# Optimization experiments

Hardware: AMD Instinct MI355X
Metric: run time of the kernel (lower is better)

The kernel has to match this reference:

```python
import jax, jax.numpy as jnp
import numpy as np

B, E, S = 2, 1024, 2048
H = 16
D_QK = D_V = D_OUT = 1024
NEG = -1e4


def setup_inputs() -> dict:
    key = jax.random.key(0)
    ks = jax.random.split(key, 12)
    q = jax.random.normal(ks[0], (B, E, 1, S), jnp.float32)
    k = jax.random.normal(ks[1], (B, E, 1, S), jnp.float32)
    v = jax.random.normal(ks[2], (B, E, 1, S), jnp.float32)
    # causal qk_mask: (B, src, 1, tgt); src index > tgt index is masked
    causal = jnp.where(jnp.arange(S)[:, None] > jnp.arange(S)[None, :], NEG, 0.0).astype(jnp.float32)
    qk_mask = jnp.broadcast_to(causal[None, :, None, :], (B, S, 1, S))
    k_mask = jnp.zeros((B, S, 1, 1), jnp.float32)
    sc = 1.0 / np.sqrt(E)
    Wq = jax.random.normal(ks[3], (D_QK, E), jnp.float32) * sc
    Wk = jax.random.normal(ks[4], (D_QK, E), jnp.float32) * sc
    Wv = jax.random.normal(ks[5], (D_V, E), jnp.float32) * sc
    Wo = jax.random.normal(ks[6], (D_OUT, D_V), jnp.float32) * sc
    bq = jnp.zeros((D_QK,), jnp.float32)
    bk = jnp.zeros((D_QK,), jnp.float32)
    bv = jnp.zeros((D_V,), jnp.float32)
    bo = jnp.zeros((D_OUT,), jnp.float32)
    return {"q": q, "k": k, "v": v, "qk_mask": qk_mask, "k_mask": k_mask,
            "Wq": Wq, "bq": bq, "Wk": Wk, "bk": bk, "Wv": Wv, "bv": bv,
            "Wo": Wo, "bo": bo}


def reference(q, k, v, qk_mask, k_mask, Wq, bq, Wk, bk, Wv, bv, Wo, bo):
    b, _, _, tq = q.shape
    sk = k.shape[3]
    d_qk, d_v = Wq.shape[0], Wv.shape[0]
    dh, dvh = d_qk // H, d_v // H
    fact = float(dh) ** (-0.5)
    # 1x1 conv projections on (B, C, 1, S) == matmul over channels
    qp = jnp.einsum('oc,bcis->bois', Wq, q) + bq[None, :, None, None]
    kp = jnp.einsum('oc,bcis->bois', Wk, k) + bk[None, :, None, None]
    vp = jnp.einsum('oc,bcis->bois', Wv, v) + bv[None, :, None, None]
    # split heads: channel dim is head-major (contiguous chunks)
    qh = qp[:, :, 0, :].reshape(b, H, dh, tq)
    kh = kp[:, :, 0, :].reshape(b, H, dh, sk)
    vh = vp[:, :, 0, :].reshape(b, H, dvh, sk)
    # scores: (B, H, src, tgt); masks broadcast over heads
    scores = jnp.einsum('bhcq,bhck->bhkq', qh, kh) * fact
    scores = scores + qk_mask[:, None, :, 0, :] + k_mask[:, None, :, 0, 0][..., None]
    w = jax.nn.softmax(scores, axis=2)  # softmax over src (k) axis
    attn = jnp.einsum('bhkq,bhck->bhcq', w, vh).reshape(b, d_v, 1, tq)
    out = jnp.einsum('oc,bcis->bois', Wo, attn) + bo[None, :, None, None]
    return out
```

## Files before the change

### kernel.cpp

```cpp
#include <hip/hip_runtime.h>
#include <hip/hip_bf16.h>
#include <stdint.h>

typedef unsigned short u16;
typedef __attribute__((ext_vector_type(8))) short short8;
typedef __attribute__((ext_vector_type(4))) short short4v;
typedef __attribute__((ext_vector_type(4))) float f32x4;

#define MFMA16(a,b,c) __builtin_amdgcn_mfma_f32_16x16x32_bf16((a),(b),(c),0,0,0)
#define EXP2F(x) __builtin_amdgcn_exp2f(x)

typedef const __attribute__((address_space(1))) void glb_void;
typedef __attribute__((address_space(3))) void lds_void;

__device__ __forceinline__ u16 f2b(float f){
  unsigned u = __float_as_uint(f);
  u += 0x7fffu + ((u>>16)&1u);
  return (u16)(u>>16);
}
__device__ __forceinline__ unsigned pack_bf16(float a, float b){
  __hip_bfloat162 h = __float22bfloat162_rn(make_float2(a,b));
  unsigned u; __builtin_memcpy(&u, &h, 4); return u;
}
__device__ __forceinline__ void gld16(const void* g, void* l){
  __builtin_amdgcn_global_load_lds((glb_void*)g, (lds_void*)l, 16, 0, 0);
}

__device__ __forceinline__ void stage128x64_sw(const u16* g, u16* lds, int gstride, int w, int lane){
  const int sub = lane>>3, c16 = lane&7;
  const int gcol = (c16 ^ sub)<<3;
  #pragma unroll
  for (int i=0;i<4;++i){
    int r0 = (w*4+i)*8;
    gld16(g + (size_t)(r0 + sub)*gstride + gcol, lds + r0*64);
  }
}
__device__ __forceinline__ void stage64x64_sw(const u16* g, u16* lds, int gstride, int w, int lane){
  const int sub = lane>>3, c16 = lane&7;
  const int gcol = (c16 ^ sub)<<3;
  #pragma unroll
  for (int i=0;i<2;++i){
    int r0 = (w*2+i)*8;
    gld16(g + (size_t)(r0 + sub)*gstride + gcol, lds + r0*64);
  }
}
__device__ __forceinline__ const short8* frag64(const u16* lds, int row, int c16){
  return (const short8*)(lds + row*64 + ((c16 ^ (row&7))<<3));
}
__device__ __forceinline__ const short8* frag128(const u16* lds, int row, int c16){
  return (const short8*)(lds + row*128 + ((c16 ^ (row&15))<<3));
}

__global__ __launch_bounds__(256) void prep(
    const float* __restrict__ q, const float* __restrict__ k, const float* __restrict__ v,
    const float* __restrict__ qkm, const float* __restrict__ km,
    const float* __restrict__ Wq, const float* __restrict__ Wk,
    const float* __restrict__ Wv, const float* __restrict__ Wo,
    u16* __restrict__ W16, char* __restrict__ classes,
    u16* __restrict__ qT, u16* __restrict__ kT, u16* __restrict__ vT)
{
  __shared__ __align__(16) float t[64][72];
  const int bx = blockIdx.x, tid = threadIdx.x;
  const int S = 2048, E = 1024, nW = E*E;

  if (bx < 2048){
    const int sel = bx>>9, blk = bx&511;
    const float* src = sel==0?Wq : sel==1?Wk : sel==2?Wv : Wo;
    const float sc = (sel==0) ? 0.18033688f : 1.0f;
    u16* dst = W16 + (size_t)sel*nW;
    int i = (blk*256 + tid)*8;
    float4 a = *(const float4*)(src+i);
    float4 b = *(const float4*)(src+i+4);
    short8 o;
    o[0]=(short)f2b(a.x*sc); o[1]=(short)f2b(a.y*sc); o[2]=(short)f2b(a.z*sc); o[3]=(short)f2b(a.w*sc);
    o[4]=(short)f2b(b.x*sc); o[5]=(short)f2b(b.y*sc); o[6]=(short)f2b(b.z*sc); o[7]=(short)f2b(b.w*sc);
    *(short8*)(dst+i) = o;
  } else if (bx < 4096){
    const int tt = bx - 2048;
    const int b = tt>>10, qi = (tt>>5)&31, ki = tt&31;
    const int k0 = ki*64, q0 = qi*64;
    int az = 1, an = 1;
    #pragma unroll
    for (int p=0;p<4;++p){
      int e = tid + p*256;
      int row = e>>4, c4 = (e&15)*4;
      float kmv = km[(size_t)b*S + k0 + row];
      float4 mv = *(const float4*)&qkm[((size_t)b*S + k0 + row)*S + q0 + c4];
      mv.x += kmv; mv.y += kmv; mv.z += kmv; mv.w += kmv;
      az &= (mv.x==0.f) & (mv.y==0.f) & (mv.z==0.f) & (mv.w==0.f);
      an &= (mv.x<-1e3f) & (mv.y<-1e3f) & (mv.z<-1e3f) & (mv.w<-1e3f);
    }
    const int az_all = __syncthreads_and(az);
    const int an_all = __syncthreads_and(an);
    if (tid==0)
      classes[((size_t)b*32 + qi)*32 + ki] = an_all ? 2 : (az_all ? 0 : 1);
  } else {
    const int tt = bx - 4096;
    const int tensor = tt>>10, r = tt&1023;
    const int b = r>>9, rr = r&511;
    const int c0 = (rr>>5)*64, s0 = (rr&31)*64;
    const float* x = tensor==0 ? q : tensor==1 ? k : v;
    u16* xt = tensor==0 ? qT : tensor==1 ? kT : vT;
    #pragma unroll
    for (int p=0;p<4;++p){
      int e = tid + p*256;
      int row = e>>4, c4 = (e&15)*4;
      *(float4*)&t[row][c4] = *(const float4*)&x[((size_t)b*E + c0 + row)*S + s0 + c4];
    }
    __syncthreads();
    #pragma unroll
    for (int p=0;p<2;++p){
      int e = tid + p*256;
      int row = e>>3, col8 = (e&7)*8;
      short8 o;
      #pragma unroll
      for (int u=0;u<8;++u) o[u] = (short)f2b(t[col8+u][row]);
      *(short8*)&xt[((size_t)b*S + s0 + row)*E + c0 + col8] = o;
    }
  }
}

template<bool F32OUT>
__device__ __forceinline__ void gemm_core(
    const u16* __restrict__ A, const u16* __restrict__ Bt, const float* __restrict__ bias,
    float bscale, void* __restrict__ Cv, size_t cbase, int N, int K, int bias_on_m,
    int m0, int n0, u16* As, u16* Bs)
{
  const int tid = threadIdx.x, w = tid>>6, lane = tid&63;
  const int ln = lane&15, quad = lane>>4;
  const int m0w = (w>>1)*64, n0w = (w&1)*64;
  f32x4 acc[4][4];
  #pragma unroll
  for(int i=0;i<4;++i)
    #pragma unroll
    for(int j=0;j<4;++j) acc[i][j] = f32x4{0.f,0.f,0.f,0.f};

  for (int kc=0; kc<K; kc+=64){
    __syncthreads();
    stage128x64_sw(A  + (size_t)m0*K + kc, As, K, w, lane);
    stage128x64_sw(Bt + (size_t)n0*K + kc, Bs, K, w, lane);
    __syncthreads();
    #pragma unroll
    for (int kk=0; kk<64; kk+=32){
      const int c16 = (kk>>3) + quad;
      short8 af[4], bf[4];
      #pragma unroll
      for (int mt=0;mt<4;++mt) af[mt] = *frag64(As, m0w+mt*16+ln, c16);
      #pragma unroll
      for (int nt=0;nt<4;++nt) bf[nt] = *frag64(Bs, n0w+nt*16+ln, c16);
      #pragma unroll
      for (int mt=0;mt<4;++mt)
        #pragma unroll
        for (int nt=0;nt<4;++nt)
          acc[mt][nt] = MFMA16(af[mt], bf[nt], acc[mt][nt]);
    }
  }
  #pragma unroll
  for (int mt=0;mt<4;++mt){
    #pragma unroll
    for (int nt=0;nt<4;++nt){
      const int col = n0 + n0w + nt*16 + ln;
      const float bn = bias_on_m ? 0.f : bias[col]*bscale;
      #pragma unroll
      for (int r=0;r<4;++r){
        const int row = m0 + m0w + mt*16 + quad*4 + r;
        const float bb = bias_on_m ? bias[row]*bscale : bn;
        const float val = acc[mt][nt][r] + bb;
        const size_t idx = cbase + (size_t)row*N + col;
        if (F32OUT) ((float*)Cv)[idx] = val;
        else        ((u16*)Cv)[idx]   = f2b(val);
      }
    }
  }
}

__global__ __launch_bounds__(256,3) void proj(
    const u16* __restrict__ qT, const u16* __restrict__ kT, const u16* __restrict__ vT,
    const u16* __restrict__ W16,
    const float* __restrict__ bq, const float* __restrict__ bk, const float* __restrict__ bv,
    u16* __restrict__ Qb, u16* __restrict__ Kb, u16* __restrict__ Vb)
{
  __shared__ __align__(16) u16 As[128*64];
  __shared__ __align__(16) u16 Bs[128*64];
  const int bx = blockIdx.x;
  const int zone = bx>>7, r = bx&127;
  const size_t sSE = (size_t)2048*1024;
  const int nW = 1024*1024;
  if (zone < 4){
    const int sel = zone>>1, b = zone&1;
    const int m0 = (r>>3)*128, n0 = (r&7)*128;
    gemm_core<false>((sel? kT : qT) + b*sSE, W16 + (size_t)sel*nW, sel? bk : bq,
                     sel? 1.0f : 0.18033688f, sel? Kb : Qb, b*sSE,
                     1024, 1024, 0, m0, n0, As, Bs);
  } else {
    const int b = zone&1;
    const int m0 = (r>>4)*128, n0 = (r&15)*128;
    gemm_core<false>(W16 + (size_t)2*nW, vT + b*sSE, bv,
                     1.0f, Vb, b*sSE,
                     2048, 1024, 1, m0, n0, As, Bs);
  }
}

__global__ __launch_bounds__(256,4) void gemm_out64(
    const u16* __restrict__ Wo16, const u16* __restrict__ At, const float* __restrict__ bo,
    float* __restrict__ out)
{
  __shared__ __align__(16) u16 As[64*64];
  __shared__ __align__(16) u16 Bs[128*64];
  const int b = blockIdx.z;
  const int m0 = blockIdx.y*64, n0 = blockIdx.x*128;
  const size_t sSE = (size_t)2048*1024;
  const int K = 1024, N = 2048;
  const u16* Bt = At + b*sSE;
  const int tid = threadIdx.x, w = tid>>6, lane = tid&63;
  const int ln = lane&15, quad = lane>>4;
  const int m0w = (w>>1)*32, n0w = (w&1)*64;
  f32x4 acc[2][4];
  #pragma unroll
  for(int i=0;i<2;++i)
    #pragma unroll
    for(int j=0;j<4;++j) acc[i][j] = f32x4{0.f,0.f,0.f,0.f};

  for (int kc=0; kc<K; kc+=64){
    __syncthreads();
    stage64x64_sw (Wo16 + (size_t)m0*K + kc, As, K, w, lane);
    stage128x64_sw(Bt   + (size_t)n0*K + kc, Bs, K, w, lane);
    __syncthreads();
    #pragma unroll
    for (int kk=0; kk<64; kk+=32){
      const int c16 = (kk>>3) + quad;
      short8 af[2], bf[4];
      #pragma unroll
      for (int mt=0;mt<2;++mt) af[mt] = *frag64(As, m0w+mt*16+ln, c16);
      #pragma unroll
      for (int nt=0;nt<4;++nt) bf[nt] = *frag64(Bs, n0w+nt*16+ln, c16);
      #pragma unroll
      for (int mt=0;mt<2;++mt)
        #pragma unroll
        for (int nt=0;nt<4;++nt)
          acc[mt][nt] = MFMA16(af[mt], bf[nt], acc[mt][nt]);
    }
  }
  #pragma unroll
  for (int mt=0;mt<2;++mt){
    #pragma unroll
    for (int nt=0;nt<4;++nt){
      const int col = n0 + n0w + nt*16 + ln;
      #pragma unroll
      for (int r=0;r<4;++r){
        const int row = m0 + m0w + mt*16 + quad*4 + r;
        out[b*sSE + (size_t)row*N + col] = acc[mt][nt][r] + bo[row];
      }
    }
  }
}

__global__ __launch_bounds__(512,4) void attn(
    const u16* __restrict__ Qb, const u16* __restrict__ Kb, const u16* __restrict__ Vb,
    const float* __restrict__ qk_mask, const float* __restrict__ k_mask,
    const char* __restrict__ classes, u16* __restrict__ Ot)
{
  __shared__ __align__(16) u16 Ks[128*64];
  __shared__ __align__(16) u16 Vs[64*128];
  const int x = blockIdx.x;
  const int b = x&1, h = (x>>1)&15;
  const int pp = x>>5, pair = pp>>1, half = pp&1;
  const int tid = threadIdx.x, w = tid>>6, lane = tid&63;
  const int group = w>>2, wq = w&3;
  const int ln = lane&15, quad = lane>>4;
  const int S = 2048;
  const float LOG2E = 1.44269504f, C2 = 16.0f;

  const int qtA = 15-pair, qtB = pair;
  const int qt = group ? qtB : qtA;
  const int qg = qt*128 + half*64 + wq*16 + ln;
  short8 qf[2];
  #pragma unroll
  for (int kkI=0;kkI<2;++kkI)
    qf[kkI] = *(const short8*)&Qb[((size_t)b*S + qg)*1024 + h*64 + kkI*32 + quad*8];

  const char* clA = classes + ((size_t)b*32 + qtA*2 + half)*32;
  const char* clB = classes + ((size_t)b*32 + qtB*2 + half)*32;
  const char* cl  = group ? clB : clA;

  unsigned mA=0, mB=0;
  #pragma unroll
  for (int kt=0;kt<16;++kt){
    if (!((clA[2*kt]==2) & (clA[2*kt+1]==2))) mA |= 1u<<kt;
    if (!((clB[2*kt]==2) & (clB[2*kt+1]==2))) mB |= 1u<<kt;
  }
  const unsigned mS = mA|mB;
  const unsigned mMe = group ? mB : mA;

  float rs = 0.f;
  f32x4 acc[4];
  #pragma unroll
  for (int ct=0;ct<4;++ct) acc[ct] = f32x4{0.f,0.f,0.f,0.f};

  const u16* gK = Kb + ((size_t)b*S)*1024 + h*64;
  const u16* gV = Vb + ((size_t)b*1024 + h*64)*S;
  const int subK = lane>>3, cK = ((lane&7)^subK)<<3;
  const int subV = lane>>4, cV0 = lane&15;

  short8 kreg[2], vreg[2];
  auto issue = [&](int kt){
    const int k0 = kt*128;
    #pragma unroll
    for (int i=0;i<2;++i){
      const int r = (w*2+i)*8 + subK;
      kreg[i] = *(const short8*)(gK + (size_t)(k0 + r)*1024 + cK);
    }
    #pragma unroll
    for (int i=0;i<2;++i){
      const int row = (w*2+i)*4 + subV;
      vreg[i] = *(const short8*)(gV + (size_t)row*S + k0 + ((cV0 ^ (row&15))<<3));
    }
  };
  auto write_lds = [&](){
    #pragma unroll
    for (int i=0;i<2;++i)
      *(short8*)&Ks[(w*2+i)*512 + lane*8] = kreg[i];
    #pragma unroll
    for (int i=0;i<2;++i)
      *(short8*)&Vs[(w*2+i)*512 + lane*8] = vreg[i];
  };

  auto compute = [&](int kt){
    const char c0 = cl[2*kt], c1 = cl[2*kt+1];
    const bool nomask = (c0|c1)==0;
    const int k0 = kt*128;
    unsigned pk[8][2];
    #pragma unroll
    for (int t=0;t<8;++t){
      f32x4 s = f32x4{0.f,0.f,0.f,0.f};
      #pragma unroll
      for (int kkI=0;kkI<2;++kkI)
        s = MFMA16(*frag64(Ks, t*16+ln, kkI*4 + quad), qf[kkI], s);
      float e[4];
      if (nomask){
        #pragma unroll
        for (int r=0;r<4;++r) e[r] = EXP2F(s[r] - C2);
      } else {
        #pragma unroll
        for (int r=0;r<4;++r){
          const int kg = k0 + t*16 + quad*4 + r;
          const float m = qk_mask[((size_t)b*S + kg)*S + qg] + k_mask[(size_t)b*S + kg];
          e[r] = EXP2F(fmaf(m, LOG2E, s[r]) - C2);
        }
      }
      rs += (e[0]+e[1]) + (e[2]+e[3]);
      pk[t][0] = pack_bf16(e[0], e[1]);
      pk[t][1] = pack_bf16(e[2], e[3]);
    }
    const int srcA = (quad&1)*32 + ln, srcB = srcA + 16;
    const bool hi = (quad>>1)&1;
    #pragma unroll
    for (int c=0;c<4;++c){
      unsigned a0 = __shfl((int)pk[2*c][0],   srcA, 64);
      unsigned a1 = __shfl((int)pk[2*c][1],   srcA, 64);
      unsigned a2 = __shfl((int)pk[2*c][0],   srcB, 64);
      unsigned a3 = __shfl((int)pk[2*c][1],   srcB, 64);
      unsigned b0 = __shfl((int)pk[2*c+1][0], srcA, 64);
      unsigned b1 = __shfl((int)pk[2*c+1][1], srcA, 64);
      unsigned b2 = __shfl((int)pk[2*c+1][0], srcB, 64);
      unsigned b3 = __shfl((int)pk[2*c+1][1], srcB, 64);
      short8 pf;
      ((unsigned*)&pf)[0] = hi ? b0 : a0;
      ((unsigned*)&pf)[1] = hi ? b1 : a1;
      ((unsigned*)&pf)[2] = hi ? b2 : a2;
      ((unsigned*)&pf)[3] = hi ? b3 : a3;
      __builtin_amdgcn_s_setprio(1);
      #pragma unroll
      for (int ct=0;ct<4;++ct)
        acc[ct] = MFMA16(*frag128(Vs, ct*16+ln, c*4 + quad), pf, acc[ct]);
      __builtin_amdgcn_s_setprio(0);
    }
  };

  int cur = mS ? (__ffs(mS)-1) : 16;
  if (cur < 16) issue(cur);
  while (cur < 16){
    const unsigned above = mS & (0xfffffffeu << cur);
    const int nxt = above ? (__ffs(above)-1) : 16;
    __builtin_amdgcn_s_barrier();
    __builtin_amdgcn_sched_barrier(0);
    write_lds();
    if (nxt < 16) issue(nxt);
    asm volatile("s_waitcnt lgkmcnt(0)" ::: "memory");
    __builtin_amdgcn_s_barrier();
    __builtin_amdgcn_sched_barrier(0);
    if ((mMe>>cur)&1) compute(cur);
    cur = nxt;
  }

  rs += __shfl_xor(rs, 16, 64);
  rs += __shfl_xor(rs, 32, 64);
  const float rinv = 1.0f / rs;
  #pragma unroll
  for (int ct=0;ct<4;++ct){
    short4v o4;
    #pragma unroll
    for (int r=0;r<4;++r) o4[r] = (short)f2b(acc[ct][r] * rinv);
    *(short4v*)&Ot[((size_t)b*S + qg)*1024 + h*64 + ct*16 + quad*4] = o4;
  }
}

extern "C" void kernel_launch(void* const* d_in, const int* in_sizes, int n_in,
                              void* d_out, int out_size, void* d_ws, size_t ws_size,
                              hipStream_t stream)
{
  const float* q   = (const float*)d_in[0];
  const float* k   = (const float*)d_in[1];
  const float* v   = (const float*)d_in[2];
  const float* qkm = (const float*)d_in[3];
  const float* km  = (const float*)d_in[4];
  const float* Wq  = (const float*)d_in[5];
  const float* bq  = (const float*)d_in[6];
  const float* Wk  = (const float*)d_in[7];
  const float* bk  = (const float*)d_in[8];
  const float* Wv  = (const float*)d_in[9];
  const float* bv  = (const float*)d_in[10];
  const float* Wo  = (const float*)d_in[11];
  const float* bo  = (const float*)d_in[12];
  float* out = (float*)d_out;

  const size_t nAct = (size_t)2*2048*1024;
  const int   nW   = 1024*1024;

  u16* A0 = (u16*)d_ws;
  u16* A1 = A0 + nAct;
  u16* A2 = A1 + nAct;
  u16* A3 = A2 + nAct;
  u16* A4 = A3 + nAct;
  u16* A5 = A4 + nAct;
  u16* W16 = A5 + nAct;
  char* classes = (char*)(W16 + (size_t)4*nW);
  u16* Wo16 = W16 + (size_t)3*nW;

  dim3 blk(256);
  prep      <<<dim3(7168), blk, 0, stream>>>(q, k, v, qkm, km, Wq, Wk, Wv, Wo,
                                             W16, classes, A0, A1, A2);
  proj      <<<dim3(768),  blk, 0, stream>>>(A0, A1, A2, W16, bq, bk, bv, A3, A4, A5);
  attn      <<<dim3(512),  dim3(512), 0, stream>>>(A3, A4, A5, qkm, km, classes, A0);
  gemm_out64<<<dim3(16,16,2), blk, 0, stream>>>(Wo16, A0, bo, out);
}
```

Baseline: 258.7 us.

## Split attention into one 64-query strip per 256-thread block, heaviest first

Replaces the paired causal-balancing scheme, where a 512-thread block handled two query tiles (early and late) that shared K/V loads, with 1024 smaller 256-thread blocks. Each block handles one 64-query strip and is launched in descending order of work so the longest strips start first. Each block now loads only the K/V tiles it needs and skips the idle-wave iterations of the old paired scheme. In exchange, K/V tiles are no longer shared between paired tiles, so each thread issues twice as many loads per tile and there are more blocks to schedule.

```diff
diff --git a/kernel.cpp b/kernel.cpp
--- a/kernel.cpp
+++ b/kernel.cpp
@@ -255,42 +255,33 @@
   }
 }
 
-__global__ __launch_bounds__(512,4) void attn(
+__global__ __launch_bounds__(256,4) void attn(
     const u16* __restrict__ Qb, const u16* __restrict__ Kb, const u16* __restrict__ Vb,
     const float* __restrict__ qk_mask, const float* __restrict__ k_mask,
     const char* __restrict__ classes, u16* __restrict__ Ot)
 {
   __shared__ __align__(16) u16 Ks[128*64];
   __shared__ __align__(16) u16 Vs[64*128];
-  const int x = blockIdx.x;
-  const int b = x&1, h = (x>>1)&15;
-  const int pp = x>>5, pair = pp>>1, half = pp&1;
+  const int bx = blockIdx.x;
+  const int st = 31 - (bx>>5);
+  const int bh = bx & 31;
+  const int b = bh & 1, h = bh >> 1;
   const int tid = threadIdx.x, w = tid>>6, lane = tid&63;
-  const int group = w>>2, wq = w&3;
   const int ln = lane&15, quad = lane>>4;
   const int S = 2048;
   const float LOG2E = 1.44269504f, C2 = 16.0f;
 
-  const int qtA = 15-pair, qtB = pair;
-  const int qt = group ? qtB : qtA;
-  const int qg = qt*128 + half*64 + wq*16 + ln;
+  const int qg = st*64 + w*16 + ln;
   short8 qf[2];
   #pragma unroll
   for (int kkI=0;kkI<2;++kkI)
     qf[kkI] = *(const short8*)&Qb[((size_t)b*S + qg)*1024 + h*64 + kkI*32 + quad*8];
 
-  const char* clA = classes + ((size_t)b*32 + qtA*2 + half)*32;
-  const char* clB = classes + ((size_t)b*32 + qtB*2 + half)*32;
-  const char* cl  = group ? clB : clA;
-
-  unsigned mA=0, mB=0;
-  #pragma unroll
-  for (int kt=0;kt<16;++kt){
-    if (!((clA[2*kt]==2) & (clA[2*kt+1]==2))) mA |= 1u<<kt;
-    if (!((clB[2*kt]==2) & (clB[2*kt+1]==2))) mB |= 1u<<kt;
-  }
-  const unsigned mS = mA|mB;
-  const unsigned mMe = group ? mB : mA;
+  const char* cl = classes + ((size_t)b*32 + st)*32;
+  unsigned mMe=0;
+  #pragma unroll
+  for (int kt=0;kt<16;++kt)
+    if (!((cl[2*kt]==2) & (cl[2*kt+1]==2))) mMe |= 1u<<kt;
 
   float rs = 0.f;
   f32x4 acc[4];
@@ -302,27 +293,27 @@
   const int subK = lane>>3, cK = ((lane&7)^subK)<<3;
   const int subV = lane>>4, cV0 = lane&15;
 
-  short8 kreg[2], vreg[2];
+  short8 kreg[4], vreg[4];
   auto issue = [&](int kt){
     const int k0 = kt*128;
     #pragma unroll
-    for (int i=0;i<2;++i){
-      const int r = (w*2+i)*8 + subK;
+    for (int i=0;i<4;++i){
+      const int r = (w*4+i)*8 + subK;
       kreg[i] = *(const short8*)(gK + (size_t)(k0 + r)*1024 + cK);
     }
     #pragma unroll
-    for (int i=0;i<2;++i){
-      const int row = (w*2+i)*4 + subV;
+    for (int i=0;i<4;++i){
+      const int row = (w*4+i)*4 + subV;
       vreg[i] = *(const short8*)(gV + (size_t)row*S + k0 + ((cV0 ^ (row&15))<<3));
     }
   };
   auto write_lds = [&](){
     #pragma unroll
-    for (int i=0;i<2;++i)
-      *(short8*)&Ks[(w*2+i)*512 + lane*8] = kreg[i];
-    #pragma unroll
-    for (int i=0;i<2;++i)
-      *(short8*)&Vs[(w*2+i)*512 + lane*8] = vreg[i];
+    for (int i=0;i<4;++i)
+      *(short8*)&Ks[(w*4+i)*512 + lane*8] = kreg[i];
+    #pragma unroll
+    for (int i=0;i<4;++i)
+      *(short8*)&Vs[(w*4+i)*512 + lane*8] = vreg[i];
   };
 
   auto compute = [&](int kt){
@@ -377,10 +368,10 @@
     }
   };
 
-  int cur = mS ? (__ffs(mS)-1) : 16;
+  int cur = mMe ? (__ffs(mMe)-1) : 16;
   if (cur < 16) issue(cur);
   while (cur < 16){
-    const unsigned above = mS & (0xfffffffeu << cur);
+    const unsigned above = mMe & (0xfffffffeu << cur);
     const int nxt = above ? (__ffs(above)-1) : 16;
     __builtin_amdgcn_s_barrier();
     __builtin_amdgcn_sched_barrier(0);
@@ -389,7 +380,7 @@
     asm volatile("s_waitcnt lgkmcnt(0)" ::: "memory");
     __builtin_amdgcn_s_barrier();
     __builtin_amdgcn_sched_barrier(0);
-    if ((mMe>>cur)&1) compute(cur);
+    compute(cur);
     cur = nxt;
   }
 
@@ -441,6 +432,6 @@
   prep      <<<dim3(7168), blk, 0, stream>>>(q, k, v, qkm, km, Wq, Wk, Wv, Wo,
                                              W16, classes, A0, A1, A2);
   proj      <<<dim3(768),  blk, 0, stream>>>(A0, A1, A2, W16, bq, bk, bv, A3, A4, A5);
-  attn      <<<dim3(512),  dim3(512), 0, stream>>>(A3, A4, A5, qkm, km, classes, A0);
+  attn      <<<dim3(1024), blk, 0, stream>>>(A3, A4, A5, qkm, km, classes, A0);
   gemm_out64<<<dim3(16,16,2), blk, 0, stream>>>(Wo16, A0, bo, out);
 }
```

Result: slower. 293.0 us (+13.3%).
